# Optimization experiments

Hardware: AMD Instinct MI355X
Metric: run time of the kernel (lower is better)

The kernel has to match this reference:

```python
import jax, jax.numpy as jnp
import numpy as np

N_NODES = 100000
N_EDGES = 3200000
D = 16
L = 3


def setup_inputs() -> dict:
    key = jax.random.key(0)
    ks = jax.random.split(key, 7)
    scale = 1.0 / np.sqrt(D)
    x = jax.random.normal(ks[0], (N_NODES, D), dtype=jnp.float32)
    edge_index = jax.random.randint(ks[1], (2, N_EDGES), 0, N_NODES, dtype=jnp.int64)
    Wl = jax.random.normal(ks[2], (L, D, D), dtype=jnp.float32) * scale
    bl = jax.random.normal(ks[3], (L, D), dtype=jnp.float32) * scale
    Wr = jax.random.normal(ks[4], (L, D, D), dtype=jnp.float32) * scale
    Wlin = jax.random.normal(ks[5], (L, D, D), dtype=jnp.float32) * scale
    blin = jax.random.normal(ks[6], (L, D), dtype=jnp.float32) * scale
    return {"x": x, "edge_index": edge_index, "Wl": Wl, "bl": bl,
            "Wr": Wr, "Wlin": Wlin, "blin": blin}


def reference(x, edge_index, Wl, bl, Wr, Wlin, blin):
    src = edge_index[0]
    dst = edge_index[1]
    n = x.shape[0]
    # in-degree for mean aggregation (PyG SAGEConv aggr='mean')
    deg = jax.ops.segment_sum(jnp.ones((src.shape[0],), dtype=x.dtype), dst,
                              num_segments=n)
    denom = jnp.maximum(deg, 1.0)[:, None]  # nodes with no in-edges -> 0 agg
    for i in range(Wl.shape[0]):
        # gather source features, scatter-mean onto targets
        agg = jax.ops.segment_sum(x[src], dst, num_segments=n) / denom
        conv = agg @ Wl[i].T + bl[i] + x @ Wr[i].T  # SAGEConv: lin_l(agg)+lin_r(x)
        x = conv + x @ Wlin[i].T + blin[i]          # + Linear residual
    return x
```

## Files before the change

kernel.cpp:

```cpp
#include <hip/hip_runtime.h>

#define N_NODES 100000
#define N_EDGES 3200000
#define D 16
#define L 3

#define TILE 100
#define NB ((N_NODES + TILE - 1) / TILE)
#define CAP 3584
#define NBLK 500
#define SEG (N_EDGES / NBLK)
#define BINT 1024
#define CVTB 391
#define LT 512

__device__ __forceinline__ unsigned packbf(float a, float b) {
    unsigned ua = __float_as_uint(a); ua += 0x7FFFu + ((ua >> 16) & 1u);
    unsigned ub = __float_as_uint(b); ub += 0x7FFFu + ((ub >> 16) & 1u);
    return (ua >> 16) | (ub & 0xFFFF0000u);
}
#define BLO(u) __uint_as_float((u) << 16)
#define BHI(u) __uint_as_float((u) & 0xFFFF0000u)

__global__ __launch_bounds__(BINT) void pre_kernel(
        const float* __restrict__ x, unsigned* __restrict__ xbf,
        const int* __restrict__ src, const int* __restrict__ dst,
        int* __restrict__ cursor, unsigned* __restrict__ ebuf, int E, int n4) {
    __shared__ int lcnt[NB];
    __shared__ int ldiff[NB];
    __shared__ unsigned sorted[SEG];
    __shared__ unsigned short sbkt[SEG];
    int tid = threadIdx.x;

    if (blockIdx.x >= NBLK) {
        int t = (blockIdx.x - NBLK) * BINT + tid;
        if (t < n4) {
            float4 v = *(const float4*)(x + (size_t)t * 4);
            uint2 o; o.x = packbf(v.x, v.y); o.y = packbf(v.z, v.w);
            *(uint2*)(xbf + (size_t)t * 2) = o;
        }
        return;
    }

    for (int i = tid; i < NB; i += BINT) lcnt[i] = 0;
    __syncthreads();
    int b0 = blockIdx.x * SEG, b1 = min(E, b0 + SEG);
    for (int e = b0 + tid * 4; e < b1; e += BINT * 4) {
        int4 d4 = *(const int4*)(dst + e);
        atomicAdd(&lcnt[(unsigned)d4.x / TILE], 1);
        atomicAdd(&lcnt[(unsigned)d4.y / TILE], 1);
        atomicAdd(&lcnt[(unsigned)d4.z / TILE], 1);
        atomicAdd(&lcnt[(unsigned)d4.w / TILE], 1);
    }
    __syncthreads();
    {
        int v = (tid < NB) ? lcnt[tid] : 0;
        sorted[tid] = (unsigned)v;
        __syncthreads();
        for (int off = 1; off < BINT; off <<= 1) {
            unsigned t = (tid >= off) ? sorted[tid - off] : 0u;
            __syncthreads();
            sorted[tid] += t;
            __syncthreads();
        }
        if (tid < NB) {
            int excl = (int)sorted[tid] - v;
            int g = v ? (tid * CAP + atomicAdd(&cursor[tid], v)) : 0;
            ldiff[tid] = g - excl;
            lcnt[tid] = excl;
        }
        __syncthreads();
    }
    for (int e = b0 + tid * 4; e < b1; e += BINT * 4) {
        int4 d4 = *(const int4*)(dst + e);
        int4 s4 = *(const int4*)(src + e);
        unsigned b_; int pos;
        b_ = (unsigned)d4.x / TILE; pos = atomicAdd(&lcnt[b_], 1);
        sorted[pos] = ((unsigned)(d4.x - b_ * TILE) << 17) | (unsigned)s4.x; sbkt[pos] = (unsigned short)b_;
        b_ = (unsigned)d4.y / TILE; pos = atomicAdd(&lcnt[b_], 1);
        sorted[pos] = ((unsigned)(d4.y - b_ * TILE) << 17) | (unsigned)s4.y; sbkt[pos] = (unsigned short)b_;
        b_ = (unsigned)d4.z / TILE; pos = atomicAdd(&lcnt[b_], 1);
        sorted[pos] = ((unsigned)(d4.z - b_ * TILE) << 17) | (unsigned)s4.z; sbkt[pos] = (unsigned short)b_;
        b_ = (unsigned)d4.w / TILE; pos = atomicAdd(&lcnt[b_], 1);
        sorted[pos] = ((unsigned)(d4.w - b_ * TILE) << 17) | (unsigned)s4.w; sbkt[pos] = (unsigned short)b_;
    }
    __syncthreads();
    int nLoc = b1 - b0;
    for (int i = tid; i < nLoc; i += BINT) {
        int b_ = sbkt[i];
        ebuf[ldiff[b_] + i] = sorted[i];
    }
}

__device__ __forceinline__ void agg_xform(
    const float* __restrict__ self_f32, const unsigned* __restrict__ xbf,
    const unsigned* se2, const int* lofs, int n_loc,
    const float* sWl, const float* sWc, const float* sbc,
    float* __restrict__ xout, unsigned* __restrict__ xbf_out,
    int emit_bf, int b, int N, int tid) {
    int q = tid & 3;
    int n = b * TILE + n_loc;
    if (n >= N) return;

    int s0 = lofs[n_loc];
    int s1 = lofs[n_loc + 1];
    int deg = s1 - s0;

    int lane2 = q >> 1;
    int ho = (q & 1) * 4;

    float acc[8] = {0.f,0.f,0.f,0.f,0.f,0.f,0.f,0.f};
    float bcc[8] = {0.f,0.f,0.f,0.f,0.f,0.f,0.f,0.f};
    int i = s0;
    for (; i + 8 <= s1; i += 8) {
        unsigned p0 = se2[i + 0 + lane2] & 0x1FFFF;
        unsigned p1 = se2[i + 2 + lane2] & 0x1FFFF;
        unsigned p2 = se2[i + 4 + lane2] & 0x1FFFF;
        unsigned p3 = se2[i + 6 + lane2] & 0x1FFFF;
        uint4 g0 = *(const uint4*)(xbf + (size_t)p0 * 8 + ho);
        uint4 g1 = *(const uint4*)(xbf + (size_t)p1 * 8 + ho);
        uint4 g2 = *(const uint4*)(xbf + (size_t)p2 * 8 + ho);
        uint4 g3 = *(const uint4*)(xbf + (size_t)p3 * 8 + ho);
        acc[0] += BLO(g0.x); acc[1] += BHI(g0.x); acc[2] += BLO(g0.y); acc[3] += BHI(g0.y);
        acc[4] += BLO(g0.z); acc[5] += BHI(g0.z); acc[6] += BLO(g0.w); acc[7] += BHI(g0.w);
        bcc[0] += BLO(g1.x); bcc[1] += BHI(g1.x); bcc[2] += BLO(g1.y); bcc[3] += BHI(g1.y);
        bcc[4] += BLO(g1.z); bcc[5] += BHI(g1.z); bcc[6] += BLO(g1.w); bcc[7] += BHI(g1.w);
        acc[0] += BLO(g2.x); acc[1] += BHI(g2.x); acc[2] += BLO(g2.y); acc[3] += BHI(g2.y);
        acc[4] += BLO(g2.z); acc[5] += BHI(g2.z); acc[6] += BLO(g2.w); acc[7] += BHI(g2.w);
        bcc[0] += BLO(g3.x); bcc[1] += BHI(g3.x); bcc[2] += BLO(g3.y); bcc[3] += BHI(g3.y);
        bcc[4] += BLO(g3.z); bcc[5] += BHI(g3.z); bcc[6] += BLO(g3.w); bcc[7] += BHI(g3.w);
    }
    for (; i + 2 <= s1; i += 2) {
        unsigned p = se2[i + lane2] & 0x1FFFF;
        uint4 g = *(const uint4*)(xbf + (size_t)p * 8 + ho);
        acc[0] += BLO(g.x); acc[1] += BHI(g.x); acc[2] += BLO(g.y); acc[3] += BHI(g.y);
        acc[4] += BLO(g.z); acc[5] += BHI(g.z); acc[6] += BLO(g.w); acc[7] += BHI(g.w);
    }
    if (i < s1 && lane2 == 0) {
        unsigned p = se2[i] & 0x1FFFF;
        uint4 g = *(const uint4*)(xbf + (size_t)p * 8 + ho);
        acc[0] += BLO(g.x); acc[1] += BHI(g.x); acc[2] += BLO(g.y); acc[3] += BHI(g.y);
        acc[4] += BLO(g.z); acc[5] += BHI(g.z); acc[6] += BLO(g.w); acc[7] += BHI(g.w);
    }
    #pragma unroll
    for (int k = 0; k < 8; k++) acc[k] += bcc[k];
    #pragma unroll
    for (int k = 0; k < 8; k++) acc[k] += __shfl_xor(acc[k], 2, 4);

    int srcAbs = (tid & 63 & ~3) | (q >> 1);
    float inv = 1.0f / fmaxf((float)deg, 1.0f);
    float a[4];
    #pragma unroll
    for (int k = 0; k < 4; k++) {
        float lo = __shfl(acc[k], srcAbs);
        float hi = __shfl(acc[4 + k], srcAbs);
        a[k] = ((q & 1) ? hi : lo) * inv;
    }

    float xv[4];
    if (self_f32) {
        float4 xq = *(const float4*)(self_f32 + (size_t)n * D + q * 4);
        xv[0] = xq.x; xv[1] = xq.y; xv[2] = xq.z; xv[3] = xq.w;
    } else {
        uint2 gx = *(const uint2*)(xbf + (size_t)n * 8 + q * 2);
        xv[0] = BLO(gx.x); xv[1] = BHI(gx.x); xv[2] = BLO(gx.y); xv[3] = BHI(gx.y);
    }

    float o[4];
    #pragma unroll
    for (int j = 0; j < D; j++) {
        float p = 0.f;
        #pragma unroll
        for (int k = 0; k < 4; k++) {
            int kk = q * 4 + k;
            p += a[k] * sWl[j * D + kk] + xv[k] * sWc[j * D + kk];
        }
        p += __shfl_xor(p, 1, 4);
        p += __shfl_xor(p, 2, 4);
        if ((j >> 2) == q) o[j & 3] = p + sbc[j];
    }
    if (emit_bf) {
        uint2 ob; ob.x = packbf(o[0], o[1]); ob.y = packbf(o[2], o[3]);
        *(uint2*)(xbf_out + (size_t)n * 8 + q * 2) = ob;
    } else {
        *(float4*)(xout + (size_t)n * D + q * 4) = make_float4(o[0], o[1], o[2], o[3]);
    }
}

__global__ __launch_bounds__(LT) void layer0_kernel(
        const float* __restrict__ xin, const unsigned* __restrict__ xbf,
        unsigned* __restrict__ ebuf, const int* __restrict__ cnt,
        int* __restrict__ node_start, int* __restrict__ gperm,
        const float* __restrict__ Wl, const float* __restrict__ bl,
        const float* __restrict__ Wr, const float* __restrict__ Wlin,
        const float* __restrict__ blin,
        unsigned* __restrict__ xbf_out, int N) {
    __shared__ unsigned se[CAP];
    __shared__ unsigned se2[CAP];
    __shared__ int lcnt[TILE];
    __shared__ int sscan[TILE];
    __shared__ int lofs[TILE + 1];
    __shared__ int sdeg[TILE];
    __shared__ int perm[TILE];
    __shared__ float sWl[D * D];
    __shared__ float sWc[D * D];
    __shared__ float sbc[D];

    int tid = threadIdx.x;
    int b = blockIdx.x;
    int base = b * CAP;
    int nE = min(cnt[b], CAP);

    if (tid < D * D) { sWl[tid] = Wl[tid]; sWc[tid] = Wr[tid] + Wlin[tid]; }
    if (tid < D) sbc[tid] = bl[tid] + blin[tid];
    if (tid < TILE) lcnt[tid] = 0;
    __syncthreads();
    for (int i = tid; i < nE; i += LT) {
        unsigned p = ebuf[base + i];
        se[i] = p;
        atomicAdd(&lcnt[p >> 17], 1);
    }
    __syncthreads();
    if (tid < TILE) sscan[tid] = lcnt[tid];
    __syncthreads();
    for (int off = 1; off < TILE; off <<= 1) {
        int t = (tid < TILE && tid >= off) ? sscan[tid - off] : 0;
        __syncthreads();
        if (tid < TILE) sscan[tid] += t;
        __syncthreads();
    }
    if (tid < TILE) {
        int excl = sscan[tid] - lcnt[tid];
        lofs[tid] = excl;
        lcnt[tid] = excl;
        sdeg[tid] = sscan[tid] - excl;
        node_start[b * TILE + tid] = excl;
        if (tid == TILE - 1) lofs[TILE] = sscan[tid];
    }
    __syncthreads();
    if (tid < TILE) {
        int dm = sdeg[tid];
        int r = 0;
        for (int j = 0; j < TILE; j++) {
            int dj = sdeg[j];
            r += (dj > dm) || (dj == dm && j < tid);
        }
        perm[r] = tid;
        gperm[b * TILE + r] = tid;
    }
    for (int i = tid; i < nE; i += LT) {
        unsigned p = se[i];
        int pos = atomicAdd(&lcnt[p >> 17], 1);
        se2[pos] = p;
    }
    __syncthreads();
    for (int i = tid; i < nE; i += LT)
        ebuf[base + i] = se2[i];

    int grp = tid >> 2;
    int n_loc = (grp < TILE) ? perm[grp] : 0;
    if (grp >= TILE) return;
    agg_xform(xin, xbf, se2, lofs, n_loc, sWl, sWc, sbc,
              nullptr, xbf_out, 1, b, N, tid);
}

__global__ __launch_bounds__(LT) void layerN_kernel(
        const unsigned* __restrict__ xbf,
        const unsigned* __restrict__ ebuf, const int* __restrict__ cnt,
        const int* __restrict__ node_start, const int* __restrict__ gperm,
        const float* __restrict__ Wl, const float* __restrict__ bl,
        const float* __restrict__ Wr, const float* __restrict__ Wlin,
        const float* __restrict__ blin,
        float* __restrict__ xout, unsigned* __restrict__ xbf_out,
        int emit_bf, int N) {
    __shared__ unsigned se2[CAP];
    __shared__ int lofs[TILE + 1];
    __shared__ float sWl[D * D];
    __shared__ float sWc[D * D];
    __shared__ float sbc[D];

    int tid = threadIdx.x;
    int b = blockIdx.x;
    int base = b * CAP;
    int nE = min(cnt[b], CAP);

    if (tid < D * D) { sWl[tid] = Wl[tid]; sWc[tid] = Wr[tid] + Wlin[tid]; }
    if (tid < D) sbc[tid] = bl[tid] + blin[tid];
    if (tid < TILE) lofs[tid] = node_start[b * TILE + tid];
    if (tid == 0) lofs[TILE] = nE;
    for (int i = tid; i < nE; i += LT) se2[i] = ebuf[base + i];
    int grp = tid >> 2;
    int n_loc = (grp < TILE) ? gperm[b * TILE + grp] : 0;
    __syncthreads();

    if (grp >= TILE) return;
    agg_xform(nullptr, xbf, se2, lofs, n_loc, sWl, sWc, sbc,
              xout, xbf_out, emit_bf, b, N, tid);
}

extern "C" void kernel_launch(void* const* d_in, const int* in_sizes, int n_in,
                              void* d_out, int out_size, void* d_ws, size_t ws_size,
                              hipStream_t stream) {
    const float* x    = (const float*)d_in[0];
    const int*   ei   = (const int*)d_in[1];
    const float* Wl   = (const float*)d_in[2];
    const float* bl   = (const float*)d_in[3];
    const float* Wr   = (const float*)d_in[4];
    const float* Wlin = (const float*)d_in[5];
    const float* blin = (const float*)d_in[6];
    float* out = (float*)d_out;

    const int* src = ei;
    const int* dst = ei + N_EDGES;

    char* w = (char*)d_ws;
    unsigned* ebuf   = (unsigned*)w;  w += (size_t)NB * CAP * 4;
    unsigned* xbf0   = (unsigned*)w;  w += (size_t)N_NODES * 8 * 4;
    unsigned* xbf1   = (unsigned*)w;  w += (size_t)N_NODES * 8 * 4;
    int*   cursor    = (int*)w;       w += (size_t)NB * 4;
    int*   node_start= (int*)w;       w += (size_t)NB * TILE * 4;
    int*   gperm     = (int*)w;       w += (size_t)NB * TILE * 4;

    hipMemsetAsync(cursor, 0, (size_t)NB * 4, stream);
    pre_kernel<<<NBLK + CVTB, BINT, 0, stream>>>(
        x, xbf0, src, dst, cursor, ebuf, N_EDGES, N_NODES * D / 4);

    layer0_kernel<<<NB, LT, 0, stream>>>(
        x, xbf0, ebuf, cursor, node_start, gperm,
        Wl, bl, Wr, Wlin, blin, xbf1, N_NODES);
    layerN_kernel<<<NB, LT, 0, stream>>>(
        xbf1, ebuf, cursor, node_start, gperm,
        Wl + D * D, bl + D, Wr + D * D, Wlin + D * D, blin + D,
        nullptr, xbf0, 1, N_NODES);
    layerN_kernel<<<NB, LT, 0, stream>>>(
        xbf0, ebuf, cursor, node_start, gperm,
        Wl + 2 * D * D, bl + 2 * D, Wr + 2 * D * D, Wlin + 2 * D * D, blin + 2 * D,
        out, nullptr, 0, N_NODES);
}
```

Baseline: 202.6 us.

## Replace barrier-heavy shared-memory scans with wavefront shuffle scans and split pre-pass finer

The Hillis-Steele block scans in the bucketing pre-pass and in layer0 are replaced with wavefront shuffle scans: two elements per thread, plus a small cross-wave combine in the pre-pass. This removes many __syncthreads barriers. The pre-pass now runs twice as many blocks at half the size, with smaller per-block shared segments, which should raise occupancy. The self-feature load in agg_xform is hoisted ahead of the edge loop so its latency overlaps the gathers. The finer split adds more global cursor atomics and more scattered ebuf segments.

Result: slower. 228.7 us (+12.9%).

```diff
diff --git a/kernel.cpp b/kernel.cpp
--- a/kernel.cpp
+++ b/kernel.cpp
@@ -8,10 +8,10 @@
 #define TILE 100
 #define NB ((N_NODES + TILE - 1) / TILE)
 #define CAP 3584
-#define NBLK 500
+#define NBLK 1000
 #define SEG (N_EDGES / NBLK)
-#define BINT 1024
-#define CVTB 391
+#define BINT 512
+#define CVTB 782
 #define LT 512
 
 __device__ __forceinline__ unsigned packbf(float a, float b) {
@@ -30,6 +30,7 @@
     __shared__ int ldiff[NB];
     __shared__ unsigned sorted[SEG];
     __shared__ unsigned short sbkt[SEG];
+    __shared__ int wsum[8];
     int tid = threadIdx.x;
 
     if (blockIdx.x >= NBLK) {
@@ -54,20 +55,36 @@
     }
     __syncthreads();
     {
-        int v = (tid < NB) ? lcnt[tid] : 0;
-        sorted[tid] = (unsigned)v;
+        int lane = tid & 63, wv = tid >> 6;
+        int t2 = tid * 2;
+        int c0 = (t2 < NB) ? lcnt[t2] : 0;
+        int c1 = (t2 + 1 < NB) ? lcnt[t2 + 1] : 0;
+        int v = c0 + c1;
+        int s = v;
+        #pragma unroll
+        for (int d_ = 1; d_ < 64; d_ <<= 1) {
+            int u = __shfl_up(s, d_, 64);
+            if (lane >= d_) s += u;
+        }
+        if (lane == 63) wsum[wv] = s;
         __syncthreads();
-        for (int off = 1; off < BINT; off <<= 1) {
-            unsigned t = (tid >= off) ? sorted[tid - off] : 0u;
-            __syncthreads();
-            sorted[tid] += t;
-            __syncthreads();
-        }
-        if (tid < NB) {
-            int excl = (int)sorted[tid] - v;
-            int g = v ? (tid * CAP + atomicAdd(&cursor[tid], v)) : 0;
-            ldiff[tid] = g - excl;
-            lcnt[tid] = excl;
+        if (tid == 0) {
+            int a = 0;
+            #pragma unroll
+            for (int i = 0; i < 8; i++) { int t_ = wsum[i]; wsum[i] = a; a += t_; }
+        }
+        __syncthreads();
+        int excl = wsum[wv] + s - v;
+        if (t2 < NB) {
+            int g0 = c0 ? (t2 * CAP + atomicAdd(&cursor[t2], c0)) : 0;
+            ldiff[t2] = g0 - excl;
+            lcnt[t2] = excl;
+            int excl1 = excl + c0;
+            if (t2 + 1 < NB) {
+                int g1 = c1 ? ((t2 + 1) * CAP + atomicAdd(&cursor[t2 + 1], c1)) : 0;
+                ldiff[t2 + 1] = g1 - excl1;
+                lcnt[t2 + 1] = excl1;
+            }
         }
         __syncthreads();
     }
@@ -101,6 +118,15 @@
     int q = tid & 3;
     int n = b * TILE + n_loc;
     if (n >= N) return;
+
+    float xv[4];
+    if (self_f32) {
+        float4 xq = *(const float4*)(self_f32 + (size_t)n * D + q * 4);
+        xv[0] = xq.x; xv[1] = xq.y; xv[2] = xq.z; xv[3] = xq.w;
+    } else {
+        uint2 gx = *(const uint2*)(xbf + (size_t)n * 8 + q * 2);
+        xv[0] = BLO(gx.x); xv[1] = BHI(gx.x); xv[2] = BLO(gx.y); xv[3] = BHI(gx.y);
+    }
 
     int s0 = lofs[n_loc];
     int s1 = lofs[n_loc + 1];
@@ -157,15 +183,6 @@
         a[k] = ((q & 1) ? hi : lo) * inv;
     }
 
-    float xv[4];
-    if (self_f32) {
-        float4 xq = *(const float4*)(self_f32 + (size_t)n * D + q * 4);
-        xv[0] = xq.x; xv[1] = xq.y; xv[2] = xq.z; xv[3] = xq.w;
-    } else {
-        uint2 gx = *(const uint2*)(xbf + (size_t)n * 8 + q * 2);
-        xv[0] = BLO(gx.x); xv[1] = BHI(gx.x); xv[2] = BLO(gx.y); xv[3] = BHI(gx.y);
-    }
-
     float o[4];
     #pragma unroll
     for (int j = 0; j < D; j++) {
@@ -198,7 +215,6 @@
     __shared__ unsigned se[CAP];
     __shared__ unsigned se2[CAP];
     __shared__ int lcnt[TILE];
-    __shared__ int sscan[TILE];
     __shared__ int lofs[TILE + 1];
     __shared__ int sdeg[TILE];
     __shared__ int perm[TILE];
@@ -221,21 +237,28 @@
         atomicAdd(&lcnt[p >> 17], 1);
     }
     __syncthreads();
-    if (tid < TILE) sscan[tid] = lcnt[tid];
-    __syncthreads();
-    for (int off = 1; off < TILE; off <<= 1) {
-        int t = (tid < TILE && tid >= off) ? sscan[tid - off] : 0;
-        __syncthreads();
-        if (tid < TILE) sscan[tid] += t;
-        __syncthreads();
-    }
-    if (tid < TILE) {
-        int excl = sscan[tid] - lcnt[tid];
-        lofs[tid] = excl;
-        lcnt[tid] = excl;
-        sdeg[tid] = sscan[tid] - excl;
-        node_start[b * TILE + tid] = excl;
-        if (tid == TILE - 1) lofs[TILE] = sscan[tid];
+    if (tid < 64) {
+        int l2 = tid * 2;
+        int c0 = (l2 < TILE) ? lcnt[l2] : 0;
+        int c1 = (l2 + 1 < TILE) ? lcnt[l2 + 1] : 0;
+        int v = c0 + c1;
+        int s = v;
+        #pragma unroll
+        for (int d_ = 1; d_ < 64; d_ <<= 1) {
+            int u = __shfl_up(s, d_, 64);
+            if (tid >= d_) s += u;
+        }
+        int excl = s - v;
+        if (l2 < TILE) {
+            lofs[l2] = excl; sdeg[l2] = c0; lcnt[l2] = excl;
+            node_start[b * TILE + l2] = excl;
+            int e1 = excl + c0;
+            if (l2 + 1 < TILE) {
+                lofs[l2 + 1] = e1; sdeg[l2 + 1] = c1; lcnt[l2 + 1] = e1;
+                node_start[b * TILE + l2 + 1] = e1;
+            }
+        }
+        if (tid == 63) lofs[TILE] = s;
     }
     __syncthreads();
     if (tid < TILE) {
@@ -258,9 +281,8 @@
         ebuf[base + i] = se2[i];
 
     int grp = tid >> 2;
-    int n_loc = (grp < TILE) ? perm[grp] : 0;
     if (grp >= TILE) return;
-    agg_xform(xin, xbf, se2, lofs, n_loc, sWl, sWc, sbc,
+    agg_xform(xin, xbf, se2, lofs, perm[grp], sWl, sWc, sbc,
               nullptr, xbf_out, 1, b, N, tid);
 }
 
```
